# Kernel tuning notes

Measured on AMD Instinct MI355X. Metric: run time of the kernel, lower is better.

Reference implementation:

```python
import jax, jax.numpy as jnp
import numpy as np

B, Hm, Wm, Dm = 1, 32, 32, 32
N = Hm * Wm * Dm
C = 128
HEADS, DH = 8, 16
G = 32
L = 2
OUT = 1


def _ln(x, g, b):
    mu = jnp.mean(x, -1, keepdims=True)
    var = jnp.mean((x - mu) ** 2, -1, keepdims=True)
    return (x - mu) * jax.lax.rsqrt(var + 1e-5) * g + b


def setup_inputs() -> dict:
    key = jax.random.key(0)
    ks = iter(jax.random.split(key, 64))
    def nrm(shape, s=0.02):
        return jax.random.normal(next(ks), shape, jnp.float32) * s
    return {
        "x": jax.random.normal(next(ks), (B, N, 3), jnp.float32),
        "fx": jax.random.normal(next(ks), (B, N, 1), jnp.float32),
        "pre_w1": nrm((4, 2 * C)), "pre_b1": jnp.zeros((2 * C,), jnp.float32),
        "pre_w2": nrm((2 * C, C)), "pre_b2": jnp.zeros((C,), jnp.float32),
        "placeholder": jax.random.uniform(next(ks), (C,), jnp.float32) / C,
        "ln1_g": jnp.ones((L, C), jnp.float32), "ln1_b": jnp.zeros((L, C), jnp.float32),
        "convx_w": nrm((L, C, C, 3, 3, 3)), "convx_b": jnp.zeros((L, C), jnp.float32),
        "convfx_w": nrm((L, C, C, 3, 3, 3)), "convfx_b": jnp.zeros((L, C), jnp.float32),
        "slice_w": nrm((L, DH, G), 0.1), "slice_b": jnp.zeros((L, G), jnp.float32),
        "temperature": jnp.full((L, 1, HEADS, 1, 1), 0.5, jnp.float32),
        "wq": nrm((L, DH, DH), 0.1), "wk": nrm((L, DH, DH), 0.1), "wv": nrm((L, DH, DH), 0.1),
        "wo": nrm((L, HEADS * DH, C)), "bo": jnp.zeros((L, C), jnp.float32),
        "ln2_g": jnp.ones((L, C), jnp.float32), "ln2_b": jnp.zeros((L, C), jnp.float32),
        "mlp_w1": nrm((L, C, C)), "mlp_b1": jnp.zeros((L, C), jnp.float32),
        "mlp_w2": nrm((L, C, C)), "mlp_b2": jnp.zeros((L, C), jnp.float32),
        "ln3_g": jnp.ones((C,), jnp.float32), "ln3_b": jnp.zeros((C,), jnp.float32),
        "out_w": nrm((C, OUT)), "out_b": jnp.zeros((OUT,), jnp.float32),
    }


def _conv3d(x, w, b):
    # x: [B,C,H,W,D], w: [O,I,3,3,3], SAME padding (kernel//2) as torch Conv3d
    y = jax.lax.conv_general_dilated(x, w, (1, 1, 1), "SAME",
                                     dimension_numbers=("NCDHW", "OIDHW", "NCDHW"))
    return y + b[None, :, None, None, None]


def _physics_attn(z, cw_x, cb_x, cw_fx, cb_fx, sw, sb, temp, wq, wk, wv, wo, bo):
    # z: [B, N, C] -> structured mesh conv projections -> slice attention
    xg = z.reshape(B, Hm, Wm, Dm, C).transpose(0, 4, 1, 2, 3)  # [B,C,H,W,D]

    def split_heads(t):  # [B,I,H,W,D] -> [B,heads,N,dh]
        return t.transpose(0, 2, 3, 4, 1).reshape(B, N, HEADS, DH).transpose(0, 2, 1, 3)

    x_mid = split_heads(_conv3d(xg, cw_x, cb_x))
    fx_mid = split_heads(_conv3d(xg, cw_fx, cb_fx))
    # slice assignment weights: [B,heads,N,G], temperature-scaled softmax
    slice_logits = (x_mid @ sw + sb) / temp
    swt = jax.nn.softmax(slice_logits, axis=-1)
    norm = jnp.sum(swt, axis=2)  # [B,heads,G]
    tok = jnp.einsum("bhnc,bhng->bhgc", fx_mid, swt) / (norm + 1e-5)[..., None]
    q, k, v = tok @ wq, tok @ wk, tok @ wv  # [B,heads,G,dh]
    attn = jax.nn.softmax((q @ k.transpose(0, 1, 3, 2)) * (DH ** -0.5), axis=-1)
    ot = attn @ v  # [B,heads,G,dh]
    out = jnp.einsum("bhgc,bhng->bhnc", ot, swt)  # de-slice back to tokens
    out = out.transpose(0, 2, 1, 3).reshape(B, N, HEADS * DH)
    return out @ wo + bo


def reference(x, fx, pre_w1, pre_b1, pre_w2, pre_b2, placeholder,
              ln1_g, ln1_b, convx_w, convx_b, convfx_w, convfx_b,
              slice_w, slice_b, temperature, wq, wk, wv, wo, bo,
              ln2_g, ln2_b, mlp_w1, mlp_b1, mlp_w2, mlp_b2,
              ln3_g, ln3_b, out_w, out_b):
    h = jnp.concatenate([x, fx], axis=-1)  # [B,N,space+fun]
    z = jax.nn.gelu(h @ pre_w1 + pre_b1, approximate=False) @ pre_w2 + pre_b2 + placeholder
    for l in range(L):
        zn = _ln(z, ln1_g[l], ln1_b[l])
        z = _physics_attn(zn, convx_w[l], convx_b[l], convfx_w[l], convfx_b[l],
                          slice_w[l], slice_b[l], temperature[l],
                          wq[l], wk[l], wv[l], wo[l], bo[l]) + z
        zn = _ln(z, ln2_g[l], ln2_b[l])
        z = jax.nn.gelu(zn @ mlp_w1[l] + mlp_b1[l], approximate=False) @ mlp_w2[l] + mlp_b2[l] + z
    return _ln(z, ln3_g, ln3_b) @ out_w + out_b
```

## Files before the change

### kernel.cpp

```cpp
#include <hip/hip_runtime.h>
#include <hip/hip_bf16.h>

#define DEV __device__ __forceinline__

constexpr int N   = 32768;
constexpr int TOTAL_IN = 2038481;

constexpr int OFF_X        = 0;
constexpr int OFF_FX       = 98304;
constexpr int OFF_PRE_W1   = 131072;
constexpr int OFF_PRE_B1   = 132096;
constexpr int OFF_PRE_W2   = 132352;
constexpr int OFF_PRE_B2   = 165120;
constexpr int OFF_PLACE    = 165248;
constexpr int OFF_LN1_G    = 165376;
constexpr int OFF_LN1_B    = 165632;
constexpr int OFF_CONVX_W  = 165888;
constexpr int OFF_CONVX_B  = 1050624;
constexpr int OFF_CONVFX_W = 1050880;
constexpr int OFF_CONVFX_B = 1935616;
constexpr int OFF_SLICE_W  = 1935872;
constexpr int OFF_SLICE_B  = 1936896;
constexpr int OFF_TEMP     = 1936960;
constexpr int OFF_WQ       = 1936976;
constexpr int OFF_WK       = 1937488;
constexpr int OFF_WV       = 1938000;
constexpr int OFF_WO       = 1938512;
constexpr int OFF_BO       = 1971280;
constexpr int OFF_LN2_G    = 1971536;
constexpr int OFF_LN2_B    = 1971792;
constexpr int OFF_MLP_W1   = 1972048;
constexpr int OFF_MLP_B1   = 2004816;
constexpr int OFF_MLP_W2   = 2005072;
constexpr int OFF_MLP_B2   = 2037840;
constexpr int OFF_LN3_G    = 2038096;
constexpr int OFF_LN3_B    = 2038224;
constexpr int OFF_OUT_W    = 2038352;
constexpr int OFF_OUT_B    = 2038480;

__device__ __constant__ int d_PRE[32] = {
  0, 98304, 131072, 132096, 132352, 165120, 165248, 165376, 165632,
  165888, 1050624, 1050880, 1935616, 1935872, 1936896, 1936960, 1936976,
  1937488, 1938000, 1938512, 1971280, 1971536, 1971792, 1972048, 2004816,
  2005072, 2037840, 2038096, 2038224, 2038352, 2038480, 2038481
};

constexpr int CVT_A = 165888;
constexpr int CVT_B = CVT_A + 256;
constexpr int CVT_TOTAL = CVT_B + (TOTAL_IN - OFF_CONVFX_B);

constexpr size_t F_IN   = 16;
constexpr size_t F_WT   = 2038512;
constexpr size_t F_Z    = F_WT   + 1769472;
constexpr size_t F_ZN   = F_Z    + 4194304;
constexpr size_t F_CONV = F_ZN   + 4194304;
constexpr size_t F_SWT  = F_CONV + 8388608;
constexpr size_t F_TOKP = F_SWT  + 8388608;
constexpr size_t F_TOK2 = F_TOKP + 1114112;
constexpr size_t F_WP   = F_TOK2 + 34816;
constexpr size_t F_END  = F_WP   + 65536;

struct InPtrs { const void* p[31]; };

typedef short short8v  __attribute__((ext_vector_type(8)));
typedef float float4v  __attribute__((ext_vector_type(4)));
#define MFMA16(A,B,C) __builtin_amdgcn_mfma_f32_16x16x32_bf16(A,B,C,0,0,0)

DEV float geluf(float x) { return 0.5f * x * (1.0f + erff(x * 0.70710678118654752f)); }
DEV short f2bs(float x) { union { __hip_bfloat16 h; short s; } c; c.h = __float2bfloat16(x); return c.s; }
DEV float bs2f(short s) { union { unsigned u; float f; } c; c.u = ((unsigned)(unsigned short)s) << 16; return c.f; }

__global__ void k_setup(InPtrs ptrs, float* __restrict__ ws,
                        short* __restrict__ wtf, short* __restrict__ wp) {
  __shared__ short wl[13952];
  const bool isbf = (*(const unsigned*)ptrs.p[15] == 0x3F003F00u);
  int b = blockIdx.x, tid = threadIdx.x;
  if (b < 128) {
    int stride = 128 * 256;
    for (int idx = b * 256 + tid; idx < CVT_TOTAL; idx += stride) {
      int e = (idx < CVT_A) ? idx
            : (idx < CVT_B) ? (OFF_CONVX_B + (idx - CVT_A))
                            : (OFF_CONVFX_B + (idx - CVT_B));
      int lo = 0, hi = 30;
#pragma unroll
      for (int it = 0; it < 5; ++it) {
        int mid = (lo + hi + 1) >> 1;
        if (e >= d_PRE[mid]) lo = mid; else hi = mid - 1;
      }
      int loc = e - d_PRE[lo];
      float v;
      if (isbf) {
        unsigned short u = ((const unsigned short*)ptrs.p[lo])[loc];
        v = __uint_as_float(((unsigned)u) << 16);
      } else {
        v = ((const float*)ptrs.p[lo])[loc];
      }
      ws[F_IN + e] = v;
    }
  } else if (b < 256) {
    int idx = b - 128;
    int layer = idx >> 6, rem = idx & 63;
    int icb = rem >> 4, ntile = rem & 15;
    for (int i = tid; i < 13824; i += 256) {
      int oc_r = i / 864, off = i - oc_r * 864;
      int oc = ntile * 16 + oc_r;
      const void* cw = (oc < 128) ? ptrs.p[9] : ptrs.p[11];
      size_t base = ((size_t)(layer * 128 + (oc & 127)) * 128 + icb * 32) * 27 + off;
      wl[oc_r * 872 + off] = isbf ? (short)((const unsigned short*)cw)[base]
                                  : f2bs(((const float*)cw)[base]);
    }
    __syncthreads();
    int wv = tid >> 6, lane = tid & 63;
    int m = lane & 15, q = lane >> 4;
    for (int tg = 0; tg < 7; ++tg) {
      int tap = tg * 4 + wv;
      if (tap < 27) {
        short8v out;
#pragma unroll
        for (int j = 0; j < 8; ++j) out[j] = wl[m * 872 + (q * 8 + j) * 27 + tap];
        size_t f = ((size_t)((layer * 108 + icb * 27 + tap) * 16 + ntile)) * 64 + lane;
        *(short8v*)(wtf + f * 8) = out;
      }
    }
  } else {
    int f = (b - 256) * 256 + tid;
    int lane = f & 63;
    int t = f >> 6;
    const void* srcb; size_t soff; int kt, nt;
    if (t < 64) { srcb = ptrs.p[4]; soff = 0; kt = t >> 3; nt = t & 7; }
    else {
      int r = t - 64, l = r / 96, r2 = r - l * 96;
      int which = r2 >> 5, idx2 = r2 & 31;
      kt = idx2 >> 3; nt = idx2 & 7;
      srcb = (which == 0 ? ptrs.p[23] : (which == 1 ? ptrs.p[25] : ptrs.p[19]));
      soff = (size_t)l * 16384;
    }
    int k0 = kt * 32 + (lane >> 4) * 8;
    int n = nt * 16 + (lane & 15);
    size_t base = soff + (size_t)k0 * 128 + n;
    short8v out;
    if (isbf) {
      const unsigned short* src = (const unsigned short*)srcb + base;
#pragma unroll
      for (int j = 0; j < 8; ++j) out[j] = (short)src[(size_t)j * 128];
    } else {
      const float* src = (const float*)srcb + base;
#pragma unroll
      for (int j = 0; j < 8; ++j) out[j] = f2bs(src[(size_t)j * 128]);
    }
    *(short8v*)(wp + (size_t)f * 8) = out;
  }
}

__global__ __launch_bounds__(256)
void k_prenet(const float* __restrict__ ip, const short* __restrict__ wp,
              float* __restrict__ z, short* __restrict__ znb) {
  __shared__ float w1s[1024], b1s[256], cvec[128], g1s[128], be1s[128];
  __shared__ float xv[64][4];
  __shared__ __align__(16) short ts[64 * 264];
  int tid = threadIdx.x;
  int wv = tid >> 6, lane = tid & 63;
  int m = lane & 15, q = lane >> 4;
  int n0 = blockIdx.x * 64;
  for (int i = tid; i < 1024; i += 256) w1s[i] = ip[OFF_PRE_W1 + i];
  b1s[tid] = ip[OFF_PRE_B1 + tid];
  if (tid < 128) {
    cvec[tid] = ip[OFF_PRE_B2 + tid] + ip[OFF_PLACE + tid];
    g1s[tid]  = ip[OFF_LN1_G + tid];
    be1s[tid] = ip[OFF_LN1_B + tid];
  }
  if (tid < 64) {
    xv[tid][0] = ip[OFF_X + (n0 + tid) * 3 + 0];
    xv[tid][1] = ip[OFF_X + (n0 + tid) * 3 + 1];
    xv[tid][2] = ip[OFF_X + (n0 + tid) * 3 + 2];
    xv[tid][3] = ip[OFF_FX + n0 + tid];
  }
  __syncthreads();
  {
    float w0 = w1s[tid], wA = w1s[256 + tid], wB = w1s[512 + tid], wC = w1s[768 + tid];
    float bb = b1s[tid];
    for (int t = 0; t < 64; ++t) {
      float hv = bb + xv[t][0] * w0 + xv[t][1] * wA + xv[t][2] * wB + xv[t][3] * wC;
      ts[t * 264 + tid] = f2bs(geluf(hv));
    }
  }
  __syncthreads();
  const short8v* pwf = (const short8v*)wp;
  float4v acc[8];
#pragma unroll
  for (int nt = 0; nt < 8; ++nt) acc[nt] = (float4v){0.f, 0.f, 0.f, 0.f};
  for (int kt = 0; kt < 8; ++kt) {
    short8v A = *(const short8v*)(ts + (wv * 16 + m) * 264 + kt * 32 + q * 8);
#pragma unroll
    for (int nt = 0; nt < 8; ++nt)
      acc[nt] = MFMA16(A, pwf[(kt * 8 + nt) * 64 + lane], acc[nt]);
  }
  float vz[8][4];
#pragma unroll
  for (int nt = 0; nt < 8; ++nt) {
    int col = nt * 16 + m;
#pragma unroll
    for (int r = 0; r < 4; ++r) {
      vz[nt][r] = acc[nt][r] + cvec[col];
      z[(size_t)(n0 + wv * 16 + q * 4 + r) * 128 + col] = vz[nt][r];
    }
  }
#pragma unroll
  for (int r = 0; r < 4; ++r) {
    float s1 = 0.f, s2 = 0.f;
#pragma unroll
    for (int nt = 0; nt < 8; ++nt) { float v = vz[nt][r]; s1 += v; s2 += v * v; }
#pragma unroll
    for (int off = 1; off < 16; off <<= 1) { s1 += __shfl_xor(s1, off); s2 += __shfl_xor(s2, off); }
    float mu = s1 * (1.0f / 128.0f);
    float var = s2 * (1.0f / 128.0f) - mu * mu;
    float rst = 1.0f / sqrtf(var + 1e-5f);
    size_t rowb = (size_t)(n0 + wv * 16 + q * 4 + r) * 128;
#pragma unroll
    for (int nt = 0; nt < 8; ++nt) {
      int col = nt * 16 + m;
      znb[rowb + col] = f2bs((vz[nt][r] - mu) * rst * g1s[col] + be1s[col]);
    }
  }
}

__global__ __launch_bounds__(256)
void k_conv(const float* __restrict__ ip, const short* __restrict__ znb,
            const short* __restrict__ wtf, short* __restrict__ cvb, int layer) {
  __shared__ __align__(16) short halo[15360];
  int tid = threadIdx.x;
  int wv = tid >> 6, lane = tid & 63;
  int m = lane & 15, q = lane >> 4;
  int n0 = blockIdx.x * 64;
  int h = n0 >> 10, w0 = (n0 >> 5) & 31;
  float bias_r[4];
#pragma unroll
  for (int nt = 0; nt < 4; ++nt) {
    int oc = (wv * 4 + nt) * 16 + m;
    bias_r[nt] = (oc < 128) ? ip[OFF_CONVX_B + layer * 128 + oc]
                            : ip[OFF_CONVFX_B + layer * 128 + (oc - 128)];
  }
  float4v acc[4][4];
#pragma unroll
  for (int a = 0; a < 4; ++a)
#pragma unroll
    for (int b = 0; b < 4; ++b) acc[a][b] = (float4v){0.f, 0.f, 0.f, 0.f};

  const short8v* wf = (const short8v*)wtf + (size_t)layer * 110592 + (wv * 4) * 64 + lane;
  short8v bc0 = wf[0], bc1 = wf[64], bc2 = wf[128], bc3 = wf[192];

  int tap = 0, icb = 0;
  for (int kt = 0; kt < 108; ++kt) {
    if (tap == 0) {
      __syncthreads();
      for (int i = tid; i < 1632; i += 256) {
        int pr = i >> 2, qq = i & 3;
        int line = pr / 34, dpos = pr - line * 34;
        int hh2 = h + (line >> 2) - 1, ww2 = w0 + (line & 3) - 1, dd2 = dpos - 1;
        short8v v = (short8v){0, 0, 0, 0, 0, 0, 0, 0};
        if (((unsigned)hh2 < 32u) && ((unsigned)ww2 < 32u) && ((unsigned)dd2 < 32u)) {
          int tok = (hh2 << 10) + (ww2 << 5) + dd2;
          v = *(const short8v*)(znb + (size_t)tok * 128 + icb * 32 + qq * 8);
        }
        *(short8v*)(halo + qq * 3840 + (line * 40 + dpos) * 8) = v;
      }
      __syncthreads();
    }
    int ktn = (kt + 1 < 108) ? kt + 1 : kt;
    const short8v* wn = wf + (size_t)ktn * 1024;
    short8v bn0 = wn[0], bn1 = wn[64], bn2 = wn[128], bn3 = wn[192];

    int ta = tap / 9, rem = tap - ta * 9, tb = rem / 3, tc = rem - tb * 3;
    const short* hp = halo + q * 3840 + ((ta * 4 + tb) * 40 + tc + m) * 8;
    short8v A0 = *(const short8v*)(hp);
    short8v A1 = *(const short8v*)(hp + 128);
    short8v A2 = *(const short8v*)(hp + 320);
    short8v A3 = *(const short8v*)(hp + 448);

    acc[0][0] = MFMA16(A0, bc0, acc[0][0]);
    acc[1][0] = MFMA16(A1, bc0, acc[1][0]);
    acc[2][0] = MFMA16(A2, bc0, acc[2][0]);
    acc[3][0] = MFMA16(A3, bc0, acc[3][0]);
    acc[0][1] = MFMA16(A0, bc1, acc[0][1]);
    acc[1][1] = MFMA16(A1, bc1, acc[1][1]);
    acc[2][1] = MFMA16(A2, bc1, acc[2][1]);
    acc[3][1] = MFMA16(A3, bc1, acc[3][1]);
    acc[0][2] = MFMA16(A0, bc2, acc[0][2]);
    acc[1][2] = MFMA16(A1, bc2, acc[1][2]);
    acc[2][2] = MFMA16(A2, bc2, acc[2][2]);
    acc[3][2] = MFMA16(A3, bc2, acc[3][2]);
    acc[0][3] = MFMA16(A0, bc3, acc[0][3]);
    acc[1][3] = MFMA16(A1, bc3, acc[1][3]);
    acc[2][3] = MFMA16(A2, bc3, acc[2][3]);
    acc[3][3] = MFMA16(A3, bc3, acc[3][3]);

    bc0 = bn0; bc1 = bn1; bc2 = bn2; bc3 = bn3;
    if (++tap == 27) { tap = 0; ++icb; }
  }
#pragma unroll
  for (int mt = 0; mt < 4; ++mt) {
    short* cp = cvb + (size_t)(n0 + mt * 16 + q * 4) * 256 + (wv * 4) * 16 + m;
#pragma unroll
    for (int nt = 0; nt < 4; ++nt) {
#pragma unroll
      for (int r = 0; r < 4; ++r)
        cp[(size_t)r * 256 + nt * 16] = f2bs(acc[mt][nt][r] + bias_r[nt]);
    }
  }
}

__global__ __launch_bounds__(256)
void k_slice(const float* __restrict__ ip, const short* __restrict__ cvb,
             short* __restrict__ swtb, float* __restrict__ tokp, int layer) {
  __shared__ float sws[512], sbs[32], its[8];
  __shared__ float swl[32 * 257];
  __shared__ __align__(16) short fxl[32 * 132];
  int tid = threadIdx.x;
  for (int i = tid; i < 512; i += 256) sws[i] = ip[OFF_SLICE_W + layer * 512 + i];
  if (tid < 32) sbs[tid] = ip[OFF_SLICE_B + layer * 32 + tid];
  if (tid < 8)  its[tid] = 1.0f / ip[OFF_TEMP + layer * 8 + tid];
  float4 ta0 = make_float4(0,0,0,0), ta1 = ta0, ta2 = ta0, ta3 = ta0;
  float np = 0.f;
  for (int s = 0; s < 4; ++s) {
    int tbase = blockIdx.x * 128 + s * 32;
    __syncthreads();
    for (int i = tid; i < 512; i += 256) {
      int t = i >> 4, c8 = (i & 15) * 8;
      *(short8v*)(fxl + t * 132 + c8) = *(const short8v*)(cvb + (size_t)(tbase + t) * 256 + 128 + c8);
    }
    {
      int t = tid >> 3, hh = tid & 7;
      float xm[16];
      short8v x0 = *(const short8v*)(cvb + (size_t)(tbase + t) * 256 + hh * 16);
      short8v x1 = *(const short8v*)(cvb + (size_t)(tbase + t) * 256 + hh * 16 + 8);
#pragma unroll
      for (int j = 0; j < 8; ++j) { xm[j] = bs2f(x0[j]); xm[8 + j] = bs2f(x1[j]); }
      float lg[32];
      float itv = its[hh];
#pragma unroll
      for (int g = 0; g < 32; ++g) {
        float sacc = sbs[g];
#pragma unroll
        for (int j = 0; j < 16; ++j) sacc += xm[j] * sws[j * 32 + g];
        lg[g] = sacc * itv;
      }
      float mx = -1e30f;
#pragma unroll
      for (int g = 0; g < 32; ++g) mx = fmaxf(mx, lg[g]);
      float sum = 0.f;
#pragma unroll
      for (int g = 0; g < 32; ++g) { lg[g] = expf(lg[g] - mx); sum += lg[g]; }
      float inv = 1.0f / sum;
#pragma unroll
      for (int g = 0; g < 32; ++g) {
        lg[g] *= inv;
        swl[t * 257 + hh * 32 + g] = lg[g];
      }
#pragma unroll
      for (int qq = 0; qq < 4; ++qq) {
        short8v pk;
#pragma unroll
        for (int j = 0; j < 8; ++j) pk[j] = f2bs(lg[qq * 8 + j]);
        *(short8v*)(swtb + (size_t)(tbase + t) * 256 + hh * 32 + qq * 8) = pk;
      }
    }
    __syncthreads();
    {
      int ah = tid >> 5, ag = tid & 31;
      for (int t2 = 0; t2 < 32; ++t2) {
        float sv = swl[t2 * 257 + ah * 32 + ag];
        np += sv;
        short8v f0 = *(const short8v*)(fxl + t2 * 132 + ah * 16);
        short8v f1 = *(const short8v*)(fxl + t2 * 132 + ah * 16 + 8);
        ta0.x += sv * bs2f(f0[0]); ta0.y += sv * bs2f(f0[1]); ta0.z += sv * bs2f(f0[2]); ta0.w += sv * bs2f(f0[3]);
        ta1.x += sv * bs2f(f0[4]); ta1.y += sv * bs2f(f0[5]); ta1.z += sv * bs2f(f0[6]); ta1.w += sv * bs2f(f0[7]);
        ta2.x += sv * bs2f(f1[0]); ta2.y += sv * bs2f(f1[1]); ta2.z += sv * bs2f(f1[2]); ta2.w += sv * bs2f(f1[3]);
        ta3.x += sv * bs2f(f1[4]); ta3.y += sv * bs2f(f1[5]); ta3.z += sv * bs2f(f1[6]); ta3.w += sv * bs2f(f1[7]);
      }
    }
  }
  int ah = tid >> 5, ag = tid & 31;
  size_t base = (size_t)blockIdx.x * 4352 + (size_t)(ah * 32 + ag) * 16;
  *(float4*)&tokp[base + 0]  = ta0;
  *(float4*)&tokp[base + 4]  = ta1;
  *(float4*)&tokp[base + 8]  = ta2;
  *(float4*)&tokp[base + 12] = ta3;
  tokp[(size_t)blockIdx.x * 4352 + 4096 + ah * 32 + ag] = np;
}

__global__ void k_tokred1(const float* __restrict__ tokp, float* __restrict__ tok2) {
  int ogrp = blockIdx.x % 17, bgrp = blockIdx.x / 17;
  int o = ogrp * 256 + threadIdx.x;
  float s = 0.f;
  int b0 = bgrp * 32;
#pragma unroll 8
  for (int b = b0; b < b0 + 32; ++b) s += tokp[(size_t)b * 4352 + o];
  tok2[(size_t)bgrp * 4352 + o] = s;
}

__global__ __launch_bounds__(256)
void k_fused(const float* __restrict__ ip, const short* __restrict__ swtb,
             const float* __restrict__ tok2, const short* __restrict__ wp,
             float* __restrict__ z, short* __restrict__ znb,
             void* __restrict__ dout, const void* __restrict__ tempraw, int layer) {
  __shared__ __align__(16) char smem[64512];
  short* otb = (short*)smem;
  float* bia = (float*)(smem + 8192);
  float* trs = (float*)(smem + 12288);
  short* znt = (short*)(smem + 12288);
  float* kk  = (float*)(smem + 29696);
  short* al  = (short*)(smem + 29696);
  float* vvs = (float*)(smem + 47104);
  float* bol = bia, *b1s = bia + 128, *b2s = bia + 256, *g2s = bia + 384;
  float* be2s = bia + 512, *lng = bia + 640, *lnb = bia + 768, *ows = bia + 896;
  int tid = threadIdx.x;
  int wv = tid >> 6, lane = tid & 63;
  int m = lane & 15, q = lane >> 4;
  int n0 = blockIdx.x * 64;
  if (tid < 128) {
    bol[tid]  = ip[OFF_BO + layer * 128 + tid];
    b1s[tid]  = ip[OFF_MLP_B1 + layer * 128 + tid];
    b2s[tid]  = ip[OFF_MLP_B2 + layer * 128 + tid];
    g2s[tid]  = ip[OFF_LN2_G + layer * 128 + tid];
    be2s[tid] = ip[OFF_LN2_B + layer * 128 + tid];
    if (layer == 0) {
      lng[tid] = ip[OFF_LN1_G + 128 + tid];
      lnb[tid] = ip[OFF_LN1_B + 128 + tid];
      ows[tid] = 0.f;
    } else {
      lng[tid] = ip[OFF_LN3_G + tid];
      lnb[tid] = ip[OFF_LN3_B + tid];
      ows[tid] = ip[OFF_OUT_W + tid];
    }
  }
  for (int i = tid; i < 4352; i += 256) {
    float s = 0.f;
#pragma unroll
    for (int b = 0; b < 8; ++b) s += tok2[(size_t)b * 4352 + i];
    trs[i] = s;
  }
  __syncthreads();
  float qv[16];
  {
    const float* wqp = ip + OFF_WQ + layer * 256;
    const float* wkp = ip + OFF_WK + layer * 256;
    const float* wvp = ip + OFF_WV + layer * 256;
    float inv = 1.0f / (trs[4096 + tid] + 1e-5f);
    float t[16];
#pragma unroll
    for (int c = 0; c < 16; ++c) t[c] = trs[tid * 16 + c] * inv;
#pragma unroll
    for (int c = 0; c < 16; ++c) {
      float aq = 0.f, ak = 0.f, av = 0.f;
#pragma unroll
      for (int j = 0; j < 16; ++j) {
        float tv = t[j];
        aq += tv * wqp[j * 16 + c];
        ak += tv * wkp[j * 16 + c];
        av += tv * wvp[j * 16 + c];
      }
      qv[c] = aq;
      kk[tid * 17 + c] = ak;
      vvs[tid * 17 + c] = av;
    }
  }
  __syncthreads();
  {
    int hh = tid >> 5, g = tid & 31;
    float sc[32];
    float mx = -1e30f;
#pragma unroll
    for (int g2 = 0; g2 < 32; ++g2) {
      float s = 0.f;
#pragma unroll
      for (int c = 0; c < 16; ++c) s += qv[c] * kk[(hh * 32 + g2) * 17 + c];
      s *= 0.25f;
      sc[g2] = s; mx = fmaxf(mx, s);
    }
    float sum = 0.f;
#pragma unroll
    for (int g2 = 0; g2 < 32; ++g2) { sc[g2] = expf(sc[g2] - mx); sum += sc[g2]; }
    float inv2 = 1.0f / sum;
    float o[16];
#pragma unroll
    for (int c = 0; c < 16; ++c) o[c] = 0.f;
#pragma unroll
    for (int g2 = 0; g2 < 32; ++g2) {
      float p = sc[g2] * inv2;
#pragma unroll
      for (int c = 0; c < 16; ++c) o[c] += p * vvs[(hh * 32 + g2) * 17 + c];
    }
#pragma unroll
    for (int dh = 0; dh < 16; ++dh)
      otb[hh * 512 + (((g >> 3) * 16 + dh) << 3) + (g & 7)] = f2bs(o[dh]);
  }
  __syncthreads();
  float4v accd[8];
#pragma unroll
  for (int h = 0; h < 8; ++h) accd[h] = (float4v){0.f, 0.f, 0.f, 0.f};
#pragma unroll
  for (int h = 0; h < 8; ++h) {
    short8v A = *(const short8v*)(swtb + (size_t)(n0 + wv * 16 + m) * 256 + h * 32 + q * 8);
    accd[h] = MFMA16(A, *(const short8v*)(otb + h * 512 + lane * 8), accd[h]);
  }
  __syncthreads();
#pragma unroll
  for (int h = 0; h < 8; ++h)
#pragma unroll
    for (int r = 0; r < 4; ++r)
      al[(wv * 16 + q * 4 + r) * 136 + h * 16 + m] = f2bs(accd[h][r]);
  __syncthreads();
  const short8v* wof = (const short8v*)(wp + (size_t)(128 + 96 * layer) * 512);
  float4v a2[8];
#pragma unroll
  for (int nt = 0; nt < 8; ++nt) a2[nt] = (float4v){0.f, 0.f, 0.f, 0.f};
  for (int kt = 0; kt < 4; ++kt) {
    short8v A = *(const short8v*)(al + (wv * 16 + m) * 136 + kt * 32 + q * 8);
#pragma unroll
    for (int nt = 0; nt < 8; ++nt)
      a2[nt] = MFMA16(A, wof[(kt * 8 + nt) * 64 + lane], a2[nt]);
  }
  float vmid[8][4];
#pragma unroll
  for (int nt = 0; nt < 8; ++nt) {
    int col = nt * 16 + m;
#pragma unroll
    for (int r = 0; r < 4; ++r)
      vmid[nt][r] = z[(size_t)(n0 + wv * 16 + q * 4 + r) * 128 + col] + a2[nt][r] + bol[col];
  }
#pragma unroll
  for (int r = 0; r < 4; ++r) {
    float s1 = 0.f, s2 = 0.f;
#pragma unroll
    for (int nt = 0; nt < 8; ++nt) { float v = vmid[nt][r]; s1 += v; s2 += v * v; }
#pragma unroll
    for (int off = 1; off < 16; off <<= 1) { s1 += __shfl_xor(s1, off); s2 += __shfl_xor(s2, off); }
    float mu = s1 * (1.0f / 128.0f);
    float var = s2 * (1.0f / 128.0f) - mu * mu;
    float rst = 1.0f / sqrtf(var + 1e-5f);
#pragma unroll
    for (int nt = 0; nt < 8; ++nt) {
      int col = nt * 16 + m;
      znt[(wv * 16 + q * 4 + r) * 136 + col] = f2bs((vmid[nt][r] - mu) * rst * g2s[col] + be2s[col]);
    }
  }
  __syncthreads();
  const short8v* w1f = (const short8v*)(wp + (size_t)(64 + 96 * layer) * 512);
  const short8v* w2f = (const short8v*)(wp + (size_t)(96 + 96 * layer) * 512);
  float4v acc[8];
#pragma unroll
  for (int nt = 0; nt < 8; ++nt) acc[nt] = (float4v){0.f, 0.f, 0.f, 0.f};
  for (int kt = 0; kt < 4; ++kt) {
    short8v A = *(const short8v*)(znt + (wv * 16 + m) * 136 + kt * 32 + q * 8);
#pragma unroll
    for (int nt = 0; nt < 8; ++nt)
      acc[nt] = MFMA16(A, w1f[(kt * 8 + nt) * 64 + lane], acc[nt]);
  }
  __syncthreads();
#pragma unroll
  for (int nt = 0; nt < 8; ++nt) {
    int col = nt * 16 + m;
#pragma unroll
    for (int r = 0; r < 4; ++r)
      al[(wv * 16 + q * 4 + r) * 136 + col] = f2bs(geluf(acc[nt][r] + b1s[col]));
  }
  __syncthreads();
  float4v a4[8];
#pragma unroll
  for (int nt = 0; nt < 8; ++nt) a4[nt] = (float4v){0.f, 0.f, 0.f, 0.f};
  for (int kt = 0; kt < 4; ++kt) {
    short8v A = *(const short8v*)(al + (wv * 16 + m) * 136 + kt * 32 + q * 8);
#pragma unroll
    for (int nt = 0; nt < 8; ++nt)
      a4[nt] = MFMA16(A, w2f[(kt * 8 + nt) * 64 + lane], a4[nt]);
  }
  float vfin[8][4];
#pragma unroll
  for (int nt = 0; nt < 8; ++nt) {
    int col = nt * 16 + m;
#pragma unroll
    for (int r = 0; r < 4; ++r) {
      vfin[nt][r] = vmid[nt][r] + a4[nt][r] + b2s[col];
      z[(size_t)(n0 + wv * 16 + q * 4 + r) * 128 + col] = vfin[nt][r];
    }
  }
#pragma unroll
  for (int r = 0; r < 4; ++r) {
    float s1 = 0.f, s2 = 0.f;
#pragma unroll
    for (int nt = 0; nt < 8; ++nt) { float v = vfin[nt][r]; s1 += v; s2 += v * v; }
#pragma unroll
    for (int off = 1; off < 16; off <<= 1) { s1 += __shfl_xor(s1, off); s2 += __shfl_xor(s2, off); }
    float mu = s1 * (1.0f / 128.0f);
    float var = s2 * (1.0f / 128.0f) - mu * mu;
    float rst = 1.0f / sqrtf(var + 1e-5f);
    int n = n0 + wv * 16 + q * 4 + r;
    if (layer == 0) {
      size_t rowb = (size_t)n * 128;
#pragma unroll
      for (int nt = 0; nt < 8; ++nt) {
        int col = nt * 16 + m;
        znb[rowb + col] = f2bs((vfin[nt][r] - mu) * rst * lng[col] + lnb[col]);
      }
    } else {
      float contrib = 0.f;
#pragma unroll
      for (int nt = 0; nt < 8; ++nt) {
        int col = nt * 16 + m;
        contrib += ((vfin[nt][r] - mu) * rst * lng[col] + lnb[col]) * ows[col];
      }
#pragma unroll
      for (int off = 1; off < 16; off <<= 1) contrib += __shfl_xor(contrib, off);
      if (m == 0) {
        float res = contrib + ip[OFF_OUT_B];
        unsigned tw = *(const unsigned*)tempraw;
        if (tw == 0x3F003F00u) ((__hip_bfloat16*)dout)[n] = __float2bfloat16(res);
        else                   ((float*)dout)[n] = res;
      }
    }
  }
}

extern "C" void kernel_launch(void* const* d_in, const int* in_sizes, int n_in,
                              void* d_out, int out_size, void* d_ws, size_t ws_size,
                              hipStream_t stream) {
  (void)in_sizes; (void)out_size; (void)ws_size;
  if (n_in < 31) return;
  float* ws   = (float*)d_ws;
  float* ip   = ws + F_IN;
  short* wtf  = (short*)(ws + F_WT);
  float* z    = ws + F_Z;
  short* znb  = (short*)(ws + F_ZN);
  short* cvb  = (short*)(ws + F_CONV);
  short* swtb = (short*)(ws + F_SWT);
  float* tkp  = ws + F_TOKP;
  float* tk2  = ws + F_TOK2;
  short* wp   = (short*)(ws + F_WP);

  InPtrs P;
  for (int i = 0; i < 31; ++i) P.p[i] = d_in[i];

  k_setup <<<320, 256, 0, stream>>>(P, ws, wtf, wp);
  k_prenet<<<512, 256, 0, stream>>>(ip, wp, z, znb);
  for (int l = 0; l < 2; ++l) {
    k_conv   <<<512, 256, 0, stream>>>(ip, znb, wtf, cvb, l);
    k_slice  <<<256, 256, 0, stream>>>(ip, cvb, swtb, tkp, l);
    k_tokred1<<<136, 256, 0, stream>>>(tkp, tk2);
    k_fused  <<<512, 256, 0, stream>>>(ip, swtb, tk2, wp, z, znb, d_out, d_in[15], l);
  }
}
```

Baseline: 478.6 us.

## Hoist slice attention into a single-block kernel shared by all fused blocks

The small slice-token attention (token reduction, q/k/v projection, softmax, attn@v) used to be recomputed redundantly by every one of the 512 blocks of the fused kernel. It now runs once per layer in a separate one-block kernel that writes the bf16 attention output to the workspace, and the fused kernel only copies that result into shared memory. The fused kernel also prefetches its slice-weight MFMA operands and residual z values into registers at the start, and its shared memory shrinks. The cost is one extra launch per layer, a serial single-block kernel on the critical path, and higher register pressure from the prefetched values.

```diff
diff --git a/kernel.cpp b/kernel.cpp
--- a/kernel.cpp
+++ b/kernel.cpp
@@ -57,7 +57,8 @@
 constexpr size_t F_SWT  = F_CONV + 8388608;
 constexpr size_t F_TOKP = F_SWT  + 8388608;
 constexpr size_t F_TOK2 = F_TOKP + 1114112;
-constexpr size_t F_WP   = F_TOK2 + 34816;
+constexpr size_t F_OT   = F_TOK2 + 34816;
+constexpr size_t F_WP   = F_OT   + 2048;
 constexpr size_t F_END  = F_WP   + 65536;
 
 struct InPtrs { const void* p[31]; };
@@ -399,24 +400,102 @@
 }
 
 __global__ __launch_bounds__(256)
+void k_attn(const float* __restrict__ ip, const float* __restrict__ tok2,
+            short* __restrict__ ot, int layer) {
+  __shared__ float trs[4352];
+  __shared__ float kk[256 * 17], vvs[256 * 17];
+  int tid = threadIdx.x;
+  for (int i = tid; i < 4352; i += 256) {
+    float s = 0.f;
+#pragma unroll
+    for (int b = 0; b < 8; ++b) s += tok2[(size_t)b * 4352 + i];
+    trs[i] = s;
+  }
+  __syncthreads();
+  float qv[16];
+  {
+    const float* wqp = ip + OFF_WQ + layer * 256;
+    const float* wkp = ip + OFF_WK + layer * 256;
+    const float* wvp = ip + OFF_WV + layer * 256;
+    float inv = 1.0f / (trs[4096 + tid] + 1e-5f);
+    float t[16];
+#pragma unroll
+    for (int c = 0; c < 16; ++c) t[c] = trs[tid * 16 + c] * inv;
+#pragma unroll
+    for (int c = 0; c < 16; ++c) {
+      float aq = 0.f, ak = 0.f, av = 0.f;
+#pragma unroll
+      for (int j = 0; j < 16; ++j) {
+        float tv = t[j];
+        aq += tv * wqp[j * 16 + c];
+        ak += tv * wkp[j * 16 + c];
+        av += tv * wvp[j * 16 + c];
+      }
+      qv[c] = aq;
+      kk[tid * 17 + c] = ak;
+      vvs[tid * 17 + c] = av;
+    }
+  }
+  __syncthreads();
+  {
+    int hh = tid >> 5, g = tid & 31;
+    float sc[32];
+    float mx = -1e30f;
+#pragma unroll
+    for (int g2 = 0; g2 < 32; ++g2) {
+      float s = 0.f;
+#pragma unroll
+      for (int c = 0; c < 16; ++c) s += qv[c] * kk[(hh * 32 + g2) * 17 + c];
+      s *= 0.25f;
+      sc[g2] = s; mx = fmaxf(mx, s);
+    }
+    float sum = 0.f;
+#pragma unroll
+    for (int g2 = 0; g2 < 32; ++g2) { sc[g2] = expf(sc[g2] - mx); sum += sc[g2]; }
+    float inv2 = 1.0f / sum;
+    float o[16];
+#pragma unroll
+    for (int c = 0; c < 16; ++c) o[c] = 0.f;
+#pragma unroll
+    for (int g2 = 0; g2 < 32; ++g2) {
+      float p = sc[g2] * inv2;
+#pragma unroll
+      for (int c = 0; c < 16; ++c) o[c] += p * vvs[(hh * 32 + g2) * 17 + c];
+    }
+#pragma unroll
+    for (int dh = 0; dh < 16; ++dh)
+      ot[hh * 512 + (((g >> 3) * 16 + dh) << 3) + (g & 7)] = f2bs(o[dh]);
+  }
+}
+
+__global__ __launch_bounds__(256)
 void k_fused(const float* __restrict__ ip, const short* __restrict__ swtb,
-             const float* __restrict__ tok2, const short* __restrict__ wp,
+             const short* __restrict__ ot, const short* __restrict__ wp,
              float* __restrict__ z, short* __restrict__ znb,
              void* __restrict__ dout, const void* __restrict__ tempraw, int layer) {
-  __shared__ __align__(16) char smem[64512];
-  short* otb = (short*)smem;
-  float* bia = (float*)(smem + 8192);
-  float* trs = (float*)(smem + 12288);
-  short* znt = (short*)(smem + 12288);
-  float* kk  = (float*)(smem + 29696);
-  short* al  = (short*)(smem + 29696);
-  float* vvs = (float*)(smem + 47104);
+  __shared__ __align__(16) short otb[4096];
+  __shared__ float bia[1024];
+  __shared__ __align__(16) short znt[8704];
+  __shared__ __align__(16) short al[8704];
   float* bol = bia, *b1s = bia + 128, *b2s = bia + 256, *g2s = bia + 384;
   float* be2s = bia + 512, *lng = bia + 640, *lnb = bia + 768, *ows = bia + 896;
   int tid = threadIdx.x;
   int wv = tid >> 6, lane = tid & 63;
   int m = lane & 15, q = lane >> 4;
   int n0 = blockIdx.x * 64;
+  short8v swA[8];
+#pragma unroll
+  for (int h = 0; h < 8; ++h)
+    swA[h] = *(const short8v*)(swtb + (size_t)(n0 + wv * 16 + m) * 256 + h * 32 + q * 8);
+  float zpre[8][4];
+#pragma unroll
+  for (int nt = 0; nt < 8; ++nt) {
+    int col = nt * 16 + m;
+#pragma unroll
+    for (int r = 0; r < 4; ++r)
+      zpre[nt][r] = z[(size_t)(n0 + wv * 16 + q * 4 + r) * 128 + col];
+  }
+  for (int i = tid; i < 4096; i += 256) otb[i] = ot[i];
   if (tid < 128) {
     bol[tid]  = ip[OFF_BO + layer * 128 + tid];
     b1s[tid]  = ip[OFF_MLP_B1 + layer * 128 + tid];
@@ -433,77 +512,13 @@
       ows[tid] = ip[OFF_OUT_W + tid];
     }
   }
-  for (int i = tid; i < 4352; i += 256) {
-    float s = 0.f;
-#pragma unroll
-    for (int b = 0; b < 8; ++b) s += tok2[(size_t)b * 4352 + i];
-    trs[i] = s;
-  }
-  __syncthreads();
-  float qv[16];
-  {
-    const float* wqp = ip + OFF_WQ + layer * 256;
-    const float* wkp = ip + OFF_WK + layer * 256;
-    const float* wvp = ip + OFF_WV + layer * 256;
-    float inv = 1.0f / (trs[4096 + tid] + 1e-5f);
-    float t[16];
-#pragma unroll
-    for (int c = 0; c < 16; ++c) t[c] = trs[tid * 16 + c] * inv;
-#pragma unroll
-    for (int c = 0; c < 16; ++c) {
-      float aq = 0.f, ak = 0.f, av = 0.f;
-#pragma unroll
-      for (int j = 0; j < 16; ++j) {
-        float tv = t[j];
-        aq += tv * wqp[j * 16 + c];
-        ak += tv * wkp[j * 16 + c];
-        av += tv * wvp[j * 16 + c];
-      }
-      qv[c] = aq;
-      kk[tid * 17 + c] = ak;
-      vvs[tid * 17 + c] = av;
-    }
-  }
-  __syncthreads();
-  {
-    int hh = tid >> 5, g = tid & 31;
-    float sc[32];
-    float mx = -1e30f;
-#pragma unroll
-    for (int g2 = 0; g2 < 32; ++g2) {
-      float s = 0.f;
-#pragma unroll
-      for (int c = 0; c < 16; ++c) s += qv[c] * kk[(hh * 32 + g2) * 17 + c];
-      s *= 0.25f;
-      sc[g2] = s; mx = fmaxf(mx, s);
-    }
-    float sum = 0.f;
-#pragma unroll
-    for (int g2 = 0; g2 < 32; ++g2) { sc[g2] = expf(sc[g2] - mx); sum += sc[g2]; }
-    float inv2 = 1.0f / sum;
-    float o[16];
-#pragma unroll
-    for (int c = 0; c < 16; ++c) o[c] = 0.f;
-#pragma unroll
-    for (int g2 = 0; g2 < 32; ++g2) {
-      float p = sc[g2] * inv2;
-#pragma unroll
-      for (int c = 0; c < 16; ++c) o[c] += p * vvs[(hh * 32 + g2) * 17 + c];
-    }
-#pragma unroll
-    for (int dh = 0; dh < 16; ++dh)
-      otb[hh * 512 + (((g >> 3) * 16 + dh) << 3) + (g & 7)] = f2bs(o[dh]);
-  }
   __syncthreads();
   float4v accd[8];
 #pragma unroll
   for (int h = 0; h < 8; ++h) accd[h] = (float4v){0.f, 0.f, 0.f, 0.f};
 #pragma unroll
-  for (int h = 0; h < 8; ++h) {
-    short8v A = *(const short8v*)(swtb + (size_t)(n0 + wv * 16 + m) * 256 + h * 32 + q * 8);
-    accd[h] = MFMA16(A, *(const short8v*)(otb + h * 512 + lane * 8), accd[h]);
-  }
-  __syncthreads();
+  for (int h = 0; h < 8; ++h)
+    accd[h] = MFMA16(swA[h], *(const short8v*)(otb + h * 512 + lane * 8), accd[h]);
 #pragma unroll
   for (int h = 0; h < 8; ++h)
 #pragma unroll
@@ -526,7 +541,7 @@
     int col = nt * 16 + m;
 #pragma unroll
     for (int r = 0; r < 4; ++r)
-      vmid[nt][r] = z[(size_t)(n0 + wv * 16 + q * 4 + r) * 128 + col] + a2[nt][r] + bol[col];
+      vmid[nt][r] = zpre[nt][r] + a2[nt][r] + bol[col];
   }
 #pragma unroll
   for (int r = 0; r < 4; ++r) {
@@ -635,6 +650,7 @@
   short* swtb = (short*)(ws + F_SWT);
   float* tkp  = ws + F_TOKP;
   float* tk2  = ws + F_TOK2;
+  short* ot   = (short*)(ws + F_OT);
   short* wp   = (short*)(ws + F_WP);
 
   InPtrs P;
@@ -646,6 +662,7 @@
     k_conv   <<<512, 256, 0, stream>>>(ip, znb, wtf, cvb, l);
     k_slice  <<<256, 256, 0, stream>>>(ip, cvb, swtb, tkp, l);
     k_tokred1<<<136, 256, 0, stream>>>(tkp, tk2);
-    k_fused  <<<512, 256, 0, stream>>>(ip, swtb, tk2, wp, z, znb, d_out, d_in[15], l);
-  }
-}
+    k_attn   <<<1, 256, 0, stream>>>(ip, tk2, ot, l);
+    k_fused  <<<512, 256, 0, stream>>>(ip, swtb, ot, wp, z, znb, d_out, d_in[15], l);
+  }
+}
```

New measurement: 537.8 us. +12.4%, slower.
